# Optimization experiments

Hardware: AMD Instinct MI355X
Metric: run time of the kernel (lower is better)

The kernel has to match this reference:

```python
import jax, jax.numpy as jnp
import numpy as np

B, CH, IMG, P = 16, 3, 384, 16
D, HEADS, DH, MLP, DEPTH = 384, 6, 64, 1536, 6
INNER = HEADS * DH
PD = P * P * 5 * CH          # SPT patch dim = 3840
GRID = IMG // P              # 24
NP = GRID * GRID             # 576 patches
SEQ = NP + 1                 # +cls = 577


def layer_norm(x, g, b, eps=1e-5):
    mu = jnp.mean(x, axis=-1, keepdims=True)
    var = jnp.var(x, axis=-1, keepdims=True)
    return (x - mu) * jax.lax.rsqrt(var + eps) * g + b


def spt_shifts(x):
    # F.pad semantics: (left,right,top,bottom) with negative = crop
    s1 = jnp.pad(x, ((0, 0), (0, 0), (0, 0), (1, 0)))[:, :, :, :-1]  # (1,-1,0,0)
    s2 = jnp.pad(x, ((0, 0), (0, 0), (0, 0), (0, 1)))[:, :, :, 1:]   # (-1,1,0,0)
    s3 = jnp.pad(x, ((0, 0), (0, 0), (1, 0), (0, 0)))[:, :, :-1, :]  # (0,0,1,-1)
    s4 = jnp.pad(x, ((0, 0), (0, 0), (0, 1), (0, 0)))[:, :, 1:, :]   # (0,0,-1,1)
    return jnp.concatenate([x, s1, s2, s3, s4], axis=1)  # [b, 5c, H, W]


def patchify(x):
    # 'b c (h p1) (w p2) -> b (h w) (p1 p2 c)'
    b, c, _, _ = x.shape
    x = x.reshape(b, c, GRID, P, GRID, P)
    x = x.transpose(0, 2, 4, 3, 5, 1)  # b h w p1 p2 c
    return x.reshape(b, GRID * GRID, P * P * c)


def setup_inputs():
    key = jax.random.key(0)
    ks = jax.random.split(key, 16)
    img = jax.random.normal(ks[0], (B, CH, IMG, IMG), jnp.float32)
    spt_g = jnp.ones((PD,), jnp.float32)
    spt_b = jnp.zeros((PD,), jnp.float32)
    spt_w = jax.random.normal(ks[1], (PD, D), jnp.float32) * (1.0 / np.sqrt(PD))
    spt_bias = jnp.zeros((D,), jnp.float32)
    pos = jax.random.normal(ks[2], (1, SEQ, D), jnp.float32) * 0.02
    cls = jax.random.normal(ks[3], (1, 1, D), jnp.float32) * 0.02
    attn_g = jnp.ones((DEPTH, D), jnp.float32)
    attn_b = jnp.zeros((DEPTH, D), jnp.float32)
    temp = jnp.full((DEPTH,), np.log(DH ** -0.5), jnp.float32)
    wqkv = jax.random.normal(ks[4], (DEPTH, D, 3 * INNER), jnp.float32) * 0.02
    wout = jax.random.normal(ks[5], (DEPTH, INNER, D), jnp.float32) * 0.02
    bout = jnp.zeros((DEPTH, D), jnp.float32)
    ff_g = jnp.ones((DEPTH, D), jnp.float32)
    ff_b = jnp.zeros((DEPTH, D), jnp.float32)
    w1 = jax.random.normal(ks[6], (DEPTH, D, MLP), jnp.float32) * 0.02
    b1 = jnp.zeros((DEPTH, MLP), jnp.float32)
    w2 = jax.random.normal(ks[7], (DEPTH, MLP, D), jnp.float32) * 0.02
    b2 = jnp.zeros((DEPTH, D), jnp.float32)
    return {"img": img, "spt_g": spt_g, "spt_b": spt_b, "spt_w": spt_w,
            "spt_bias": spt_bias, "pos": pos, "cls": cls, "attn_g": attn_g,
            "attn_b": attn_b, "temp": temp, "wqkv": wqkv, "wout": wout,
            "bout": bout, "ff_g": ff_g, "ff_b": ff_b, "w1": w1, "b1": b1,
            "w2": w2, "b2": b2}


def vit_forward(img, spt_g, spt_b, spt_w, spt_bias, pos, cls, attn_g, attn_b,
                temp, wqkv, wout, bout, ff_g, ff_b, w1, b1, w2, b2):
    # SPT patch embedding
    x = patchify(spt_shifts(img))                      # [b, NP, PD]
    x = layer_norm(x, spt_g, spt_b) @ spt_w + spt_bias  # [b, NP, D]
    b = x.shape[0]
    cls_tok = jnp.broadcast_to(cls, (b, 1, D))
    x = jnp.concatenate([cls_tok, x], axis=1) + pos[:, :SEQ]

    eye = jnp.eye(SEQ, dtype=bool)
    neg = -jnp.finfo(x.dtype).max

    def block(x, p):
        ag, ab, t, wq, wo, bo, fg, fb, W1, B1, W2, B2 = p
        h = layer_norm(x, ag, ab)
        qkv = h @ wq                                   # [b, n, 3*inner]
        q, k, v = jnp.split(qkv, 3, axis=-1)
        q = q.reshape(b, SEQ, HEADS, DH).transpose(0, 2, 1, 3)
        k = k.reshape(b, SEQ, HEADS, DH).transpose(0, 2, 1, 3)
        v = v.reshape(b, SEQ, HEADS, DH).transpose(0, 2, 1, 3)
        dots = jnp.einsum('bhid,bhjd->bhij', q, k) * jnp.exp(t)
        dots = jnp.where(eye, neg, dots)               # diagonal mask (LSA)
        attn = jax.nn.softmax(dots, axis=-1)
        out = jnp.einsum('bhij,bhjd->bhid', attn, v)
        out = out.transpose(0, 2, 1, 3).reshape(b, SEQ, INNER)
        x = out @ wo + bo + x
        h = layer_norm(x, fg, fb)
        x = jax.nn.gelu(h @ W1 + B1, approximate=False) @ W2 + B2 + x
        return x, None

    params = (attn_g, attn_b, temp, wqkv, wout, bout, ff_g, ff_b, w1, b1, w2, b2)
    x, _ = jax.lax.scan(block, x, params)
    return x


def reference(img, spt_g, spt_b, spt_w, spt_bias, pos, cls, attn_g, attn_b,
              temp, wqkv, wout, bout, ff_g, ff_b, w1, b1, w2, b2):
    return vit_forward(img, spt_g, spt_b, spt_w, spt_bias, pos, cls, attn_g,
                       attn_b, temp, wqkv, wout, bout, ff_g, ff_b, w1, b1,
                       w2, b2)
```

## Files before the change

kernel.cpp:

```cpp
#include <hip/hip_runtime.h>

typedef unsigned short ushort_t;
typedef __bf16 bf16x8 __attribute__((ext_vector_type(8)));
typedef float f32x4 __attribute__((ext_vector_type(4)));

#define SEQ_ 577
#define D_ 384
#define NTOK (16 * 577)

enum { M_QKV = 0, M_OUT, M_MLP1, M_MLP2 };

__device__ inline float b2f(ushort_t u) {
    unsigned int x = ((unsigned int)u) << 16;
    float f; __builtin_memcpy(&f, &x, 4); return f;
}
__device__ inline ushort_t f2b(float f) {
    unsigned int x; __builtin_memcpy(&x, &f, 4);
    x = x + 0x7fffu + ((x >> 16) & 1u);
    return (ushort_t)(x >> 16);
}

__device__ void transpose_tile(const float* __restrict__ src,
                               ushort_t* __restrict__ dst,
                               int ldn, int ldk, int k0, int n0)
{
    __shared__ float t[64][65];
    const int tid = threadIdx.x;
    const int c = tid & 63, rr = tid >> 6;
#pragma unroll
    for (int i = 0; i < 16; i++) {
        int kl = rr + i * 4;
        t[kl][c] = src[(size_t)(k0 + kl) * ldn + n0 + c];
    }
    __syncthreads();
#pragma unroll
    for (int i = 0; i < 16; i++) {
        int nl = rr + i * 4;
        dst[(size_t)(n0 + nl) * ldk + k0 + c] = f2b(t[c][nl]);
    }
}

__global__ __launch_bounds__(256) void prep_spt_kernel(
    const float* __restrict__ w, ushort_t* __restrict__ wt)
{
    transpose_tile(w, wt, 384, 3840, blockIdx.x * 64, blockIdx.y * 64);
}

__global__ __launch_bounds__(256) void prep_all_kernel(
    const float* __restrict__ wqkv, const float* __restrict__ wout,
    const float* __restrict__ w1, const float* __restrict__ w2,
    ushort_t* __restrict__ W6)
{
    int id = blockIdx.x;
    int l = id / 432;
    int r = id - l * 432;
    ushort_t* qkv_t  = W6 + (size_t)l * 1769472;
    ushort_t* wout_t = qkv_t + 442368;
    ushort_t* w1_t   = wout_t + 147456;
    ushort_t* w2_t   = w1_t + 589824;
    const float* wq = wqkv + (size_t)l * 442368;
    const float* wo = wout + (size_t)l * 147456;
    const float* W1 = w1 + (size_t)l * 589824;
    const float* W2 = w2 + (size_t)l * 589824;
    if (r < 108) {
        int kt = r / 18, nt = r % 18;
        transpose_tile(wq, qkv_t, 1152, 384, kt * 64, nt * 64);
    } else if (r < 144) {
        r -= 108; int kt = r / 6, nt = r % 6;
        transpose_tile(wo, wout_t, 384, 384, kt * 64, nt * 64);
    } else if (r < 288) {
        r -= 144; int kt = r / 24, nt = r % 24;
        transpose_tile(W1, w1_t, 1536, 384, kt * 64, nt * 64);
    } else {
        r -= 288; int kt = r / 6, nt = r % 6;
        transpose_tile(W2, w2_t, 384, 1536, kt * 64, nt * 64);
    }
}

template <int MODE>
__global__ __launch_bounds__(256) void gemm64(
    const ushort_t* __restrict__ A, const ushort_t* __restrict__ Bt,
    ushort_t* __restrict__ Co, float* __restrict__ resid,
    const float* __restrict__ bias,
    int M, int K, int ldc)
{
    __shared__ __align__(16) ushort_t As[2][64][40];
    __shared__ __align__(16) ushort_t Bs[2][64][40];

    const int gx = gridDim.x;
    const int nwg = gx * gridDim.y;
    const int f = blockIdx.y * gx + blockIdx.x;
    const int q = nwg >> 3, rr_ = nwg & 7;
    const int xcd = f & 7, ii = f >> 3;
    const int swz = (xcd < rr_ ? xcd * (q + 1) : rr_ * (q + 1) + (xcd - rr_) * q) + ii;
    const int bx = swz % gx, by = swz / gx;

    const int tid = threadIdx.x;
    const int rowBase = by * 64;
    const int colBase = bx * 64;
    const int nk = K >> 5;
    const int lr = tid >> 2, lk = (tid & 3) * 8;
    const int wv = tid >> 6, lane = tid & 63;
    const int wm = (wv >> 1) * 32, wn = (wv & 1) * 32;
    const int m16 = lane & 15, q4 = lane >> 4, kb = q4 * 8;

    const ushort_t* pa = A + (size_t)(rowBase + lr) * K + lk;
    const ushort_t* pb = Bt + (size_t)(colBase + lr) * K + lk;

    f32x4 acc[2][2];
#pragma unroll
    for (int i = 0; i < 2; i++)
#pragma unroll
        for (int j = 0; j < 2; j++) acc[i][j] = (f32x4){0.f, 0.f, 0.f, 0.f};

    uint4 Ua, Ub, Va, Vb;
    auto gloadU = [&](int kt) {
        Ua = *(const uint4*)(pa + kt * 32);
        Ub = *(const uint4*)(pb + kt * 32);
    };
    auto gloadV = [&](int kt) {
        Va = *(const uint4*)(pa + kt * 32);
        Vb = *(const uint4*)(pb + kt * 32);
    };
    auto swriteU = [&](int buf) {
        *(uint4*)&As[buf][lr][lk] = Ua;
        *(uint4*)&Bs[buf][lr][lk] = Ub;
    };
    auto swriteV = [&](int buf) {
        *(uint4*)&As[buf][lr][lk] = Va;
        *(uint4*)&Bs[buf][lr][lk] = Vb;
    };
    auto compute = [&](int buf) {
        bf16x8 a0 = *(const bf16x8*)&As[buf][wm + m16][kb];
        bf16x8 a1 = *(const bf16x8*)&As[buf][wm + 16 + m16][kb];
        bf16x8 b0 = *(const bf16x8*)&Bs[buf][wn + m16][kb];
        bf16x8 b1 = *(const bf16x8*)&Bs[buf][wn + 16 + m16][kb];
        acc[0][0] = __builtin_amdgcn_mfma_f32_16x16x32_bf16(a0, b0, acc[0][0], 0, 0, 0);
        acc[0][1] = __builtin_amdgcn_mfma_f32_16x16x32_bf16(a0, b1, acc[0][1], 0, 0, 0);
        acc[1][0] = __builtin_amdgcn_mfma_f32_16x16x32_bf16(a1, b0, acc[1][0], 0, 0, 0);
        acc[1][1] = __builtin_amdgcn_mfma_f32_16x16x32_bf16(a1, b1, acc[1][1], 0, 0, 0);
    };

    gloadU(0);
    swriteU(0);
    gloadU(1);
    gloadV(2);
    __syncthreads();

    for (int kt = 0; kt < nk; kt += 2) {
        swriteU(1);
        if (kt + 3 < nk) gloadU(kt + 3);
        compute(0);
        __syncthreads();
        if (kt + 2 < nk) {
            swriteV(0);
            if (kt + 4 < nk) gloadV(kt + 4);
        }
        compute(1);
        __syncthreads();
    }

#pragma unroll
    for (int im = 0; im < 2; im++)
#pragma unroll
        for (int in = 0; in < 2; in++) {
            int col = colBase + wn + in * 16 + m16;
#pragma unroll
            for (int r = 0; r < 4; r++) {
                int row = rowBase + wm + im * 16 + q4 * 4 + r;
                if (row >= M) continue;
                float v = acc[im][in][r];
                if (MODE == M_QKV) {
                    Co[(size_t)row * ldc + col] = f2b(v);
                } else if (MODE == M_MLP1) {
                    float t = v + bias[col];
                    float gl = 0.5f * t * (1.0f + erff(t * 0.70710678118f));
                    Co[(size_t)row * ldc + col] = f2b(gl);
                } else {
                    size_t o = (size_t)row * ldc + col;
                    resid[o] = resid[o] + v + bias[col];
                }
            }
        }
}

__global__ __launch_bounds__(256) void gemm64_spt_split(
    const ushort_t* __restrict__ A, const ushort_t* __restrict__ Bt,
    float* __restrict__ resid, int rowOff)
{
    __shared__ __align__(16) ushort_t As[2][64][40];
    __shared__ __align__(16) ushort_t Bs[2][64][40];

    const int f = blockIdx.z * 288 + blockIdx.y * 6 + blockIdx.x;
    const int swz = (f & 7) * 144 + (f >> 3);
    const int bz = swz / 288;
    const int rem = swz - bz * 288;
    const int by = rem / 6, bx = rem - by * 6;

    const int K = 3840, nk = 30;
    const int rowBase = by * 64;
    const int colBase = bx * 64;
    const int kbase = bz * 960;

    const int tid = threadIdx.x;
    const int lr = tid >> 2, lk = (tid & 3) * 8;
    const int wv = tid >> 6, lane = tid & 63;
    const int wm = (wv >> 1) * 32, wn = (wv & 1) * 32;
    const int m16 = lane & 15, q4 = lane >> 4, kb = q4 * 8;

    const ushort_t* pa = A + (size_t)(rowBase + lr) * K + kbase + lk;
    const ushort_t* pb = Bt + (size_t)(colBase + lr) * K + kbase + lk;

    f32x4 acc[2][2];
#pragma unroll
    for (int i = 0; i < 2; i++)
#pragma unroll
        for (int j = 0; j < 2; j++) acc[i][j] = (f32x4){0.f, 0.f, 0.f, 0.f};

    uint4 Ua, Ub, Va, Vb;
    auto gloadU = [&](int kt) {
        Ua = *(const uint4*)(pa + kt * 32);
        Ub = *(const uint4*)(pb + kt * 32);
    };
    auto gloadV = [&](int kt) {
        Va = *(const uint4*)(pa + kt * 32);
        Vb = *(const uint4*)(pb + kt * 32);
    };
    auto swriteU = [&](int buf) {
        *(uint4*)&As[buf][lr][lk] = Ua;
        *(uint4*)&Bs[buf][lr][lk] = Ub;
    };
    auto swriteV = [&](int buf) {
        *(uint4*)&As[buf][lr][lk] = Va;
        *(uint4*)&Bs[buf][lr][lk] = Vb;
    };
    auto compute = [&](int buf) {
        bf16x8 a0 = *(const bf16x8*)&As[buf][wm + m16][kb];
        bf16x8 a1 = *(const bf16x8*)&As[buf][wm + 16 + m16][kb];
        bf16x8 b0 = *(const bf16x8*)&Bs[buf][wn + m16][kb];
        bf16x8 b1 = *(const bf16x8*)&Bs[buf][wn + 16 + m16][kb];
        acc[0][0] = __builtin_amdgcn_mfma_f32_16x16x32_bf16(a0, b0, acc[0][0], 0, 0, 0);
        acc[0][1] = __builtin_amdgcn_mfma_f32_16x16x32_bf16(a0, b1, acc[0][1], 0, 0, 0);
        acc[1][0] = __builtin_amdgcn_mfma_f32_16x16x32_bf16(a1, b0, acc[1][0], 0, 0, 0);
        acc[1][1] = __builtin_amdgcn_mfma_f32_16x16x32_bf16(a1, b1, acc[1][1], 0, 0, 0);
    };

    gloadU(0);
    swriteU(0);
    gloadU(1);
    gloadV(2);
    __syncthreads();

    for (int kt = 0; kt < nk; kt += 2) {
        swriteU(1);
        if (kt + 3 < nk) gloadU(kt + 3);
        compute(0);
        __syncthreads();
        if (kt + 2 < nk) {
            swriteV(0);
            if (kt + 4 < nk) gloadV(kt + 4);
        }
        compute(1);
        __syncthreads();
    }

#pragma unroll
    for (int im = 0; im < 2; im++)
#pragma unroll
        for (int in = 0; in < 2; in++) {
            int col = colBase + wn + in * 16 + m16;
#pragma unroll
            for (int r = 0; r < 4; r++) {
                int row = rowBase + wm + im * 16 + q4 * 4 + r;
                int grow = rowOff + row;
                int bb = grow / 576, p = grow - bb * 576;
                size_t o = ((size_t)(bb * SEQ_ + 1 + p)) * D_ + col;
                atomicAdd(&resid[o], acc[im][in][r]);
            }
        }
}

__global__ __launch_bounds__(256) void attn_kernel(
    const ushort_t* __restrict__ qkv, ushort_t* __restrict__ attn,
    const float* __restrict__ temp, int layer)
{
    const int qt = blockIdx.x;
    const int bh = blockIdx.y;
    const int b = bh / 6, hd = bh - b * 6;
    const int tid = threadIdx.x;
    const int wv = tid >> 6, lane = tid & 63;
    const int m16 = lane & 15, q4 = lane >> 4;
    const float sc2 = expf(temp[layer]) * 1.44269504f;

    __shared__ __align__(16) ushort_t Ks[64][72];
    __shared__ __align__(16) ushort_t Vt[64][72];
    __shared__ __align__(16) ushort_t Pw[4][16][72];

    const int qrow = qt * 64 + wv * 16 + m16;
    const int qtok = qrow < SEQ_ ? qrow : SEQ_ - 1;
    const ushort_t* qb = qkv + ((size_t)(b * SEQ_ + qtok)) * 1152 + hd * 64;
    bf16x8 qf0 = *(const bf16x8*)(qb + q4 * 8);
    bf16x8 qf1 = *(const bf16x8*)(qb + 32 + q4 * 8);

    f32x4 accO[4];
#pragma unroll
    for (int dt = 0; dt < 4; dt++) accO[dt] = (f32x4){0.f, 0.f, 0.f, 0.f};
    float l_r[4] = {0.f, 0.f, 0.f, 0.f};

    const int skey = tid >> 2;
    const int scol = (tid & 3) * 16;
    const int vp   = tid & 31;
    const int vdh  = (tid >> 5) * 8;

    for (int kt = 0; kt < 10; kt++) {
        int key = kt * 64 + skey;
        int gkey = key < SEQ_ ? key : 0;
        const ushort_t* kb_ = qkv + ((size_t)(b * SEQ_ + gkey)) * 1152 + 384 + hd * 64;
        uint4 kv0 = *(const uint4*)(kb_ + scol);
        uint4 kv1 = *(const uint4*)(kb_ + scol + 8);
        if (key >= SEQ_) { kv0 = (uint4){0, 0, 0, 0}; kv1 = kv0; }
        int vk0 = kt * 64 + 2 * vp;
        int t0 = vk0 < SEQ_ ? vk0 : 0;
        int t1 = vk0 + 1 < SEQ_ ? vk0 + 1 : 0;
        uint4 va = *(const uint4*)(qkv + ((size_t)(b * SEQ_ + t0)) * 1152 + 768 + hd * 64 + vdh);
        uint4 vb2 = *(const uint4*)(qkv + ((size_t)(b * SEQ_ + t1)) * 1152 + 768 + hd * 64 + vdh);
        if (vk0 >= SEQ_) va = (uint4){0, 0, 0, 0};
        if (vk0 + 1 >= SEQ_) vb2 = (uint4){0, 0, 0, 0};
        __syncthreads();
        *(uint4*)&Ks[skey][scol] = kv0;
        *(uint4*)&Ks[skey][scol + 8] = kv1;
        {
            const ushort_t* e0 = (const ushort_t*)&va;
            const ushort_t* e1 = (const ushort_t*)&vb2;
#pragma unroll
            for (int j = 0; j < 8; j++) {
                unsigned int pack = (unsigned int)e0[j] | ((unsigned int)e1[j] << 16);
                *(unsigned int*)&Vt[vdh + j][2 * vp] = pack;
            }
        }
        __syncthreads();

        f32x4 s[4];
#pragma unroll
        for (int ct = 0; ct < 4; ct++) {
            bf16x8 b0 = *(const bf16x8*)&Ks[ct * 16 + m16][q4 * 8];
            bf16x8 b1 = *(const bf16x8*)&Ks[ct * 16 + m16][32 + q4 * 8];
            f32x4 z = (f32x4){0.f, 0.f, 0.f, 0.f};
            z = __builtin_amdgcn_mfma_f32_16x16x32_bf16(qf0, b0, z, 0, 0, 0);
            z = __builtin_amdgcn_mfma_f32_16x16x32_bf16(qf1, b1, z, 0, 0, 0);
            s[ct] = z;
        }
        const int rowb = qt * 64 + wv * 16 + q4 * 4;
#pragma unroll
        for (int r = 0; r < 4; r++) {
            float rs = 0.f;
#pragma unroll
            for (int ct = 0; ct < 4; ct++) {
                int col = kt * 64 + ct * 16 + m16;
                float v = s[ct][r] * sc2;
                if (col >= SEQ_ || col == rowb + r) v = -1.0e30f;
                float p = __builtin_amdgcn_exp2f(v);
                s[ct][r] = p;
                rs += p;
            }
            rs += __shfl_xor(rs, 1);
            rs += __shfl_xor(rs, 2);
            rs += __shfl_xor(rs, 4);
            rs += __shfl_xor(rs, 8);
            l_r[r] += rs;
        }
#pragma unroll
        for (int ct = 0; ct < 4; ct++)
#pragma unroll
            for (int r = 0; r < 4; r++)
                Pw[wv][q4 * 4 + r][ct * 16 + m16] = f2b(s[ct][r]);
        bf16x8 pf0 = *(const bf16x8*)&Pw[wv][m16][q4 * 8];
        bf16x8 pf1 = *(const bf16x8*)&Pw[wv][m16][32 + q4 * 8];
#pragma unroll
        for (int dt = 0; dt < 4; dt++) {
            bf16x8 vb0 = *(const bf16x8*)&Vt[dt * 16 + m16][q4 * 8];
            bf16x8 vb1 = *(const bf16x8*)&Vt[dt * 16 + m16][32 + q4 * 8];
            f32x4 o = accO[dt];
            o = __builtin_amdgcn_mfma_f32_16x16x32_bf16(pf0, vb0, o, 0, 0, 0);
            o = __builtin_amdgcn_mfma_f32_16x16x32_bf16(pf1, vb1, o, 0, 0, 0);
            accO[dt] = o;
        }
    }

    const int rowb = qt * 64 + wv * 16 + q4 * 4;
#pragma unroll
    for (int r = 0; r < 4; r++) {
        int grow = rowb + r;
        if (grow >= SEQ_) continue;
        float inv = 1.f / l_r[r];
        ushort_t* op = attn + ((size_t)(b * SEQ_ + grow)) * 384 + hd * 64;
#pragma unroll
        for (int dt = 0; dt < 4; dt++)
            op[dt * 16 + m16] = f2b(accO[dt][r] * inv);
    }
}

__global__ __launch_bounds__(256) void spt_ln_kernel(
    const float* __restrict__ img, const float* __restrict__ gg,
    const float* __restrict__ bb_, ushort_t* __restrict__ Xn, int r0)
{
    int bp = r0 + blockIdx.x;
    int b = bp / 576, p = bp - b * 576;
    int ph = p / 24, pw = p - ph * 24;

    __shared__ float vals[3840];
    __shared__ float red[10];

    const int tid = threadIdx.x;
    const int p1 = tid >> 4, p2 = tid & 15;

    float s = 0.f, sq = 0.f;
#pragma unroll
    for (int plane = 0; plane < 15; plane++) {
        int g5 = plane / 3, ch = plane - g5 * 3;
        int row = ph * 16 + p1, col = pw * 16 + p2;
        if (g5 == 1) col -= 1;
        else if (g5 == 2) col += 1;
        else if (g5 == 3) row -= 1;
        else if (g5 == 4) row += 1;
        float v = 0.f;
        if (row >= 0 && row < 384 && col >= 0 && col < 384)
            v = img[((size_t)(b * 3 + ch) * 384 + row) * 384 + col];
        vals[tid * 15 + plane] = v;
        s += v; sq += v * v;
    }
#pragma unroll
    for (int off = 32; off > 0; off >>= 1) {
        s += __shfl_xor(s, off);
        sq += __shfl_xor(sq, off);
    }
    int wid = tid >> 6;
    if ((tid & 63) == 0) { red[wid] = s; red[4 + wid] = sq; }
    __syncthreads();
    if (tid == 0) {
        float S = red[0] + red[1] + red[2] + red[3];
        float Q = red[4] + red[5] + red[6] + red[7];
        float mean = S / 3840.f;
        float var = Q / 3840.f - mean * mean;
        red[8] = mean;
        red[9] = rsqrtf(var + 1e-5f);
    }
    __syncthreads();
    float mean = red[8], rstd = red[9];
#pragma unroll
    for (int i = 0; i < 15; i++) {
        int k = tid + i * 256;
        float v = (vals[k] - mean) * rstd * gg[k] + bb_[k];
        Xn[(size_t)blockIdx.x * 3840 + k] = f2b(v);
    }
}

__global__ __launch_bounds__(256) void ln_kernel(
    const float* __restrict__ x, const float* __restrict__ g,
    const float* __restrict__ b, ushort_t* __restrict__ h)
{
    int row = blockIdx.x * 4 + (threadIdx.x >> 6);
    int lane = threadIdx.x & 63;
    const float4* xr = (const float4*)(x + (size_t)row * 384);
    float4 a = xr[lane];
    float4 c = (lane < 32) ? xr[64 + lane] : make_float4(0.f, 0.f, 0.f, 0.f);
    float s = a.x + a.y + a.z + a.w + c.x + c.y + c.z + c.w;
    float sq = a.x * a.x + a.y * a.y + a.z * a.z + a.w * a.w
             + c.x * c.x + c.y * c.y + c.z * c.z + c.w * c.w;
#pragma unroll
    for (int off = 32; off > 0; off >>= 1) {
        s += __shfl_xor(s, off);
        sq += __shfl_xor(sq, off);
    }
    float mean = s / 384.f;
    float var = sq / 384.f - mean * mean;
    float rstd = rsqrtf(var + 1e-5f);
    const float4* g4 = (const float4*)g;
    const float4* b4 = (const float4*)b;
    ushort_t* hr = h + (size_t)row * 384;
    {
        float4 gv = g4[lane], bv = b4[lane];
        unsigned int lo = (unsigned int)f2b((a.x - mean) * rstd * gv.x + bv.x)
                        | ((unsigned int)f2b((a.y - mean) * rstd * gv.y + bv.y) << 16);
        unsigned int hi = (unsigned int)f2b((a.z - mean) * rstd * gv.z + bv.z)
                        | ((unsigned int)f2b((a.w - mean) * rstd * gv.w + bv.w) << 16);
        *(uint2*)&hr[lane * 4] = make_uint2(lo, hi);
    }
    if (lane < 32) {
        float4 gv = g4[64 + lane], bv = b4[64 + lane];
        unsigned int lo = (unsigned int)f2b((c.x - mean) * rstd * gv.x + bv.x)
                        | ((unsigned int)f2b((c.y - mean) * rstd * gv.y + bv.y) << 16);
        unsigned int hi = (unsigned int)f2b((c.z - mean) * rstd * gv.z + bv.z)
                        | ((unsigned int)f2b((c.w - mean) * rstd * gv.w + bv.w) << 16);
        *(uint2*)&hr[256 + lane * 4] = make_uint2(lo, hi);
    }
}

__global__ void init_x_kernel(const float* __restrict__ cls,
                              const float* __restrict__ pos,
                              const float* __restrict__ spt_bias,
                              float* __restrict__ x)
{
    int s = blockIdx.x, b = blockIdx.y, d = threadIdx.x;
    float base = (s == 0) ? cls[d] : spt_bias[d];
    x[((size_t)b * SEQ_ + s) * D_ + d] = base + pos[(size_t)s * D_ + d];
}

extern "C" void kernel_launch(void* const* d_in, const int* in_sizes, int n_in,
                              void* d_out, int out_size, void* d_ws, size_t ws_size,
                              hipStream_t stream)
{
    const float* img      = (const float*)d_in[0];
    const float* spt_g    = (const float*)d_in[1];
    const float* spt_b    = (const float*)d_in[2];
    const float* spt_w    = (const float*)d_in[3];
    const float* spt_bias = (const float*)d_in[4];
    const float* pos      = (const float*)d_in[5];
    const float* clsp     = (const float*)d_in[6];
    const float* attn_g   = (const float*)d_in[7];
    const float* attn_b   = (const float*)d_in[8];
    const float* temp     = (const float*)d_in[9];
    const float* wqkv     = (const float*)d_in[10];
    const float* wout     = (const float*)d_in[11];
    const float* bout     = (const float*)d_in[12];
    const float* ff_g     = (const float*)d_in[13];
    const float* ff_b     = (const float*)d_in[14];
    const float* w1       = (const float*)d_in[15];
    const float* b1       = (const float*)d_in[16];
    const float* w2       = (const float*)d_in[17];
    const float* b2       = (const float*)d_in[18];

    float* x = (float*)d_out;

    char* base = (char*)d_ws;
    ushort_t* qkv   = (ushort_t*)base;
    ushort_t* attn  = (ushort_t*)(base + (size_t)NTOK * 1152 * 2);
    ushort_t* Xn    = (ushort_t*)base;
    ushort_t* gbuf  = (ushort_t*)base;
    ushort_t* spt_wt = (ushort_t*)(base + 23592960);
    char* p2 = base + (size_t)NTOK * 1536 * 2;
    ushort_t* h  = (ushort_t*)p2;
    char* p3 = p2 + (size_t)NTOK * 384 * 2;
    ushort_t* W6 = (ushort_t*)p3;

    prep_all_kernel<<<2592, 256, 0, stream>>>(wqkv, wout, w1, w2, W6);
    prep_spt_kernel<<<dim3(60, 6), 256, 0, stream>>>(spt_w, spt_wt);
    init_x_kernel<<<dim3(SEQ_, 16), 384, 0, stream>>>(clsp, pos, spt_bias, x);

    for (int c = 0; c < 3; c++) {
        int r0 = c * 3072;
        spt_ln_kernel<<<3072, 256, 0, stream>>>(img, spt_g, spt_b, Xn, r0);
        gemm64_spt_split<<<dim3(6, 48, 4), 256, 0, stream>>>(Xn, spt_wt, x, r0);
    }

    for (int l = 0; l < 6; l++) {
        ushort_t* qkv_t  = W6 + (size_t)l * 1769472;
        ushort_t* wout_t = qkv_t + 442368;
        ushort_t* w1_t   = wout_t + 147456;
        ushort_t* w2_t   = w1_t + 589824;
        ln_kernel<<<NTOK / 4, 256, 0, stream>>>(x, attn_g + l * 384, attn_b + l * 384, h);
        gemm64<M_QKV><<<dim3(18, 145), 256, 0, stream>>>(
            h, qkv_t, qkv, nullptr, nullptr, NTOK, 384, 1152);
        attn_kernel<<<dim3(10, 96), 256, 0, stream>>>(qkv, attn, temp, l);
        gemm64<M_OUT><<<dim3(6, 145), 256, 0, stream>>>(
            attn, wout_t, nullptr, x, bout + l * 384, NTOK, 384, 384);
        ln_kernel<<<NTOK / 4, 256, 0, stream>>>(x, ff_g + l * 384, ff_b + l * 384, h);
        gemm64<M_MLP1><<<dim3(24, 145), 256, 0, stream>>>(
            h, w1_t, gbuf, nullptr, b1 + l * 1536, NTOK, 384, 1536);
        gemm64<M_MLP2><<<dim3(6, 145), 256, 0, stream>>>(
            gbuf, w2_t, nullptr, x, b2 + l * 384, NTOK, 1536, 384);
    }
}
```

Measured before the change: 1.202 ms.

## Fuse LayerNorm into QKV and MLP1 GEMMs by folding gamma/beta into weights

Removes the standalone LayerNorm kernels. The LN gamma is folded into the transposed weights, and beta·W is precomputed as an extra bias. Each GEMM block now computes per-row mean and rstd from the fp32 residual and normalizes the A tile while loading it, in place of reading a bf16 LN output. The exact erf GELU is also replaced by a tanh-style approximation using exp2 and rcp. The trade-off is that the A operand is read as fp32 (double the bytes) and every column block recomputes the row statistics, with some change in numerical error.

```diff
diff --git a/kernel.cpp b/kernel.cpp
--- a/kernel.cpp
+++ b/kernel.cpp
@@ -22,6 +22,7 @@
 
 __device__ void transpose_tile(const float* __restrict__ src,
                                ushort_t* __restrict__ dst,
+                               const float* __restrict__ g,
                                int ldn, int ldk, int k0, int n0)
 {
     __shared__ float t[64][65];
@@ -33,22 +34,24 @@
         t[kl][c] = src[(size_t)(k0 + kl) * ldn + n0 + c];
     }
     __syncthreads();
+    float sc = g ? g[k0 + c] : 1.0f;
 #pragma unroll
     for (int i = 0; i < 16; i++) {
         int nl = rr + i * 4;
-        dst[(size_t)(n0 + nl) * ldk + k0 + c] = f2b(t[c][nl]);
+        dst[(size_t)(n0 + nl) * ldk + k0 + c] = f2b(t[c][nl] * sc);
     }
 }
 
 __global__ __launch_bounds__(256) void prep_spt_kernel(
     const float* __restrict__ w, ushort_t* __restrict__ wt)
 {
-    transpose_tile(w, wt, 384, 3840, blockIdx.x * 64, blockIdx.y * 64);
+    transpose_tile(w, wt, nullptr, 384, 3840, blockIdx.x * 64, blockIdx.y * 64);
 }
 
 __global__ __launch_bounds__(256) void prep_all_kernel(
     const float* __restrict__ wqkv, const float* __restrict__ wout,
     const float* __restrict__ w1, const float* __restrict__ w2,
+    const float* __restrict__ attn_g, const float* __restrict__ ff_g,
     ushort_t* __restrict__ W6)
 {
     int id = blockIdx.x;
@@ -64,26 +67,52 @@
     const float* W2 = w2 + (size_t)l * 589824;
     if (r < 108) {
         int kt = r / 18, nt = r % 18;
-        transpose_tile(wq, qkv_t, 1152, 384, kt * 64, nt * 64);
+        transpose_tile(wq, qkv_t, attn_g + l * 384, 1152, 384, kt * 64, nt * 64);
     } else if (r < 144) {
         r -= 108; int kt = r / 6, nt = r % 6;
-        transpose_tile(wo, wout_t, 384, 384, kt * 64, nt * 64);
+        transpose_tile(wo, wout_t, nullptr, 384, 384, kt * 64, nt * 64);
     } else if (r < 288) {
         r -= 144; int kt = r / 24, nt = r % 24;
-        transpose_tile(W1, w1_t, 1536, 384, kt * 64, nt * 64);
+        transpose_tile(W1, w1_t, ff_g + l * 384, 1536, 384, kt * 64, nt * 64);
     } else {
         r -= 288; int kt = r / 6, nt = r % 6;
-        transpose_tile(W2, w2_t, 384, 1536, kt * 64, nt * 64);
+        transpose_tile(W2, w2_t, nullptr, 384, 1536, kt * 64, nt * 64);
+    }
+}
+
+__global__ __launch_bounds__(256) void prep_bias_kernel(
+    const float* __restrict__ wqkv, const float* __restrict__ w1,
+    const float* __restrict__ b1, const float* __restrict__ attn_b,
+    const float* __restrict__ ff_b, float* __restrict__ qb2,
+    float* __restrict__ mb2)
+{
+    int gidx = blockIdx.x * 256 + threadIdx.x;
+    if (gidx >= 6 * 2688) return;
+    int l = gidx / 2688, r = gidx - l * 2688;
+    if (r < 1152) {
+        const float* W = wqkv + (size_t)l * 442368;
+        const float* bb = attn_b + l * 384;
+        float s = 0.f;
+        for (int k = 0; k < 384; k++) s += bb[k] * W[(size_t)k * 1152 + r];
+        qb2[l * 1152 + r] = s;
+    } else {
+        int n = r - 1152;
+        const float* W = w1 + (size_t)l * 589824;
+        const float* bb = ff_b + l * 384;
+        float s = b1[l * 1536 + n];
+        for (int k = 0; k < 384; k++) s += bb[k] * W[(size_t)k * 1536 + n];
+        mb2[l * 1536 + n] = s;
     }
 }
 
 template <int MODE>
 __global__ __launch_bounds__(256) void gemm64(
-    const ushort_t* __restrict__ A, const ushort_t* __restrict__ Bt,
+    const void* __restrict__ Av, const ushort_t* __restrict__ Bt,
     ushort_t* __restrict__ Co, float* __restrict__ resid,
     const float* __restrict__ bias,
     int M, int K, int ldc)
 {
+    constexpr bool LNF = (MODE == M_QKV || MODE == M_MLP1);
     __shared__ __align__(16) ushort_t As[2][64][40];
     __shared__ __align__(16) ushort_t Bs[2][64][40];
 
@@ -99,12 +128,34 @@
     const int rowBase = by * 64;
     const int colBase = bx * 64;
     const int nk = K >> 5;
-    const int lr = tid >> 2, lk = (tid & 3) * 8;
+    const int lr = tid >> 2, lq = tid & 3, lk = lq * 8;
     const int wv = tid >> 6, lane = tid & 63;
     const int wm = (wv >> 1) * 32, wn = (wv & 1) * 32;
     const int m16 = lane & 15, q4 = lane >> 4, kb = q4 * 8;
 
-    const ushort_t* pa = A + (size_t)(rowBase + lr) * K + lk;
+    const float* paf = nullptr;
+    const ushort_t* pa = nullptr;
+    float rstd = 0.f, nc = 0.f;
+    if constexpr (LNF) {
+        int ar = rowBase + lr;
+        if (ar >= M) ar = M - 1;
+        paf = (const float*)Av + (size_t)ar * K;
+        const float4* p4 = (const float4*)(paf + lq * 96);
+        float s = 0.f, sq = 0.f;
+#pragma unroll
+        for (int i = 0; i < 24; i++) {
+            float4 v = p4[i];
+            s += v.x + v.y + v.z + v.w;
+            sq += v.x * v.x + v.y * v.y + v.z * v.z + v.w * v.w;
+        }
+        s += __shfl_xor(s, 1);  s += __shfl_xor(s, 2);
+        sq += __shfl_xor(sq, 1); sq += __shfl_xor(sq, 2);
+        float mean = s * (1.f / 384.f);
+        rstd = rsqrtf(sq * (1.f / 384.f) - mean * mean + 1e-5f);
+        nc = -mean * rstd;
+    } else {
+        pa = (const ushort_t*)Av + (size_t)(rowBase + lr) * K + lk;
+    }
     const ushort_t* pb = Bt + (size_t)(colBase + lr) * K + lk;
 
     f32x4 acc[2][2];
@@ -114,20 +165,45 @@
         for (int j = 0; j < 2; j++) acc[i][j] = (f32x4){0.f, 0.f, 0.f, 0.f};
 
     uint4 Ua, Ub, Va, Vb;
+    float4 Uaf0, Uaf1, Vaf0, Vaf1;
+    auto nrm8 = [&](float4 a, float4 b) -> bf16x8 {
+        bf16x8 r;
+        r[0] = (__bf16)fmaf(a.x, rstd, nc);
+        r[1] = (__bf16)fmaf(a.y, rstd, nc);
+        r[2] = (__bf16)fmaf(a.z, rstd, nc);
+        r[3] = (__bf16)fmaf(a.w, rstd, nc);
+        r[4] = (__bf16)fmaf(b.x, rstd, nc);
+        r[5] = (__bf16)fmaf(b.y, rstd, nc);
+        r[6] = (__bf16)fmaf(b.z, rstd, nc);
+        r[7] = (__bf16)fmaf(b.w, rstd, nc);
+        return r;
+    };
     auto gloadU = [&](int kt) {
-        Ua = *(const uint4*)(pa + kt * 32);
+        if constexpr (LNF) {
+            const float4* p = (const float4*)(paf + kt * 32 + lk);
+            Uaf0 = p[0]; Uaf1 = p[1];
+        } else {
+            Ua = *(const uint4*)(pa + kt * 32);
+        }
         Ub = *(const uint4*)(pb + kt * 32);
     };
     auto gloadV = [&](int kt) {
-        Va = *(const uint4*)(pa + kt * 32);
+        if constexpr (LNF) {
+            const float4* p = (const float4*)(paf + kt * 32 + lk);
+            Vaf0 = p[0]; Vaf1 = p[1];
+        } else {
+            Va = *(const uint4*)(pa + kt * 32);
+        }
         Vb = *(const uint4*)(pb + kt * 32);
     };
     auto swriteU = [&](int buf) {
-        *(uint4*)&As[buf][lr][lk] = Ua;
+        if constexpr (LNF) *(bf16x8*)&As[buf][lr][lk] = nrm8(Uaf0, Uaf1);
+        else               *(uint4*)&As[buf][lr][lk] = Ua;
         *(uint4*)&Bs[buf][lr][lk] = Ub;
     };
     auto swriteV = [&](int buf) {
-        *(uint4*)&As[buf][lr][lk] = Va;
+        if constexpr (LNF) *(bf16x8*)&As[buf][lr][lk] = nrm8(Vaf0, Vaf1);
+        else               *(uint4*)&As[buf][lr][lk] = Va;
         *(uint4*)&Bs[buf][lr][lk] = Vb;
     };
     auto compute = [&](int buf) {
@@ -171,10 +247,12 @@
                 if (row >= M) continue;
                 float v = acc[im][in][r];
                 if (MODE == M_QKV) {
-                    Co[(size_t)row * ldc + col] = f2b(v);
+                    Co[(size_t)row * ldc + col] = f2b(v + bias[col]);
                 } else if (MODE == M_MLP1) {
                     float t = v + bias[col];
-                    float gl = 0.5f * t * (1.0f + erff(t * 0.70710678118f));
+                    float u = t * (0.7978845608f + 0.0356774081f * t * t);
+                    float e = __builtin_amdgcn_exp2f(2.885390082f * u);
+                    float gl = t - t * __builtin_amdgcn_rcpf(e + 1.0f);
                     Co[(size_t)row * ldc + col] = f2b(gl);
                 } else {
                     size_t o = (size_t)row * ldc + col;
@@ -455,47 +533,6 @@
     }
 }
 
-__global__ __launch_bounds__(256) void ln_kernel(
-    const float* __restrict__ x, const float* __restrict__ g,
-    const float* __restrict__ b, ushort_t* __restrict__ h)
-{
-    int row = blockIdx.x * 4 + (threadIdx.x >> 6);
-    int lane = threadIdx.x & 63;
-    const float4* xr = (const float4*)(x + (size_t)row * 384);
-    float4 a = xr[lane];
-    float4 c = (lane < 32) ? xr[64 + lane] : make_float4(0.f, 0.f, 0.f, 0.f);
-    float s = a.x + a.y + a.z + a.w + c.x + c.y + c.z + c.w;
-    float sq = a.x * a.x + a.y * a.y + a.z * a.z + a.w * a.w
-             + c.x * c.x + c.y * c.y + c.z * c.z + c.w * c.w;
-#pragma unroll
-    for (int off = 32; off > 0; off >>= 1) {
-        s += __shfl_xor(s, off);
-        sq += __shfl_xor(sq, off);
-    }
-    float mean = s / 384.f;
-    float var = sq / 384.f - mean * mean;
-    float rstd = rsqrtf(var + 1e-5f);
-    const float4* g4 = (const float4*)g;
-    const float4* b4 = (const float4*)b;
-    ushort_t* hr = h + (size_t)row * 384;
-    {
-        float4 gv = g4[lane], bv = b4[lane];
-        unsigned int lo = (unsigned int)f2b((a.x - mean) * rstd * gv.x + bv.x)
-                        | ((unsigned int)f2b((a.y - mean) * rstd * gv.y + bv.y) << 16);
-        unsigned int hi = (unsigned int)f2b((a.z - mean) * rstd * gv.z + bv.z)
-                        | ((unsigned int)f2b((a.w - mean) * rstd * gv.w + bv.w) << 16);
-        *(uint2*)&hr[lane * 4] = make_uint2(lo, hi);
-    }
-    if (lane < 32) {
-        float4 gv = g4[64 + lane], bv = b4[64 + lane];
-        unsigned int lo = (unsigned int)f2b((c.x - mean) * rstd * gv.x + bv.x)
-                        | ((unsigned int)f2b((c.y - mean) * rstd * gv.y + bv.y) << 16);
-        unsigned int hi = (unsigned int)f2b((c.z - mean) * rstd * gv.z + bv.z)
-                        | ((unsigned int)f2b((c.w - mean) * rstd * gv.w + bv.w) << 16);
-        *(uint2*)&hr[256 + lane * 4] = make_uint2(lo, hi);
-    }
-}
-
 __global__ void init_x_kernel(const float* __restrict__ cls,
                               const float* __restrict__ pos,
                               const float* __restrict__ spt_bias,
@@ -539,11 +576,13 @@
     ushort_t* gbuf  = (ushort_t*)base;
     ushort_t* spt_wt = (ushort_t*)(base + 23592960);
     char* p2 = base + (size_t)NTOK * 1536 * 2;
-    ushort_t* h  = (ushort_t*)p2;
+    float* qb2 = (float*)p2;
+    float* mb2 = qb2 + 6 * 1152;
     char* p3 = p2 + (size_t)NTOK * 384 * 2;
     ushort_t* W6 = (ushort_t*)p3;
 
-    prep_all_kernel<<<2592, 256, 0, stream>>>(wqkv, wout, w1, w2, W6);
+    prep_all_kernel<<<2592, 256, 0, stream>>>(wqkv, wout, w1, w2, attn_g, ff_g, W6);
+    prep_bias_kernel<<<63, 256, 0, stream>>>(wqkv, w1, b1, attn_b, ff_b, qb2, mb2);
     prep_spt_kernel<<<dim3(60, 6), 256, 0, stream>>>(spt_w, spt_wt);
     init_x_kernel<<<dim3(SEQ_, 16), 384, 0, stream>>>(clsp, pos, spt_bias, x);
 
@@ -558,15 +597,13 @@
         ushort_t* wout_t = qkv_t + 442368;
         ushort_t* w1_t   = wout_t + 147456;
         ushort_t* w2_t   = w1_t + 589824;
-        ln_kernel<<<NTOK / 4, 256, 0, stream>>>(x, attn_g + l * 384, attn_b + l * 384, h);
         gemm64<M_QKV><<<dim3(18, 145), 256, 0, stream>>>(
-            h, qkv_t, qkv, nullptr, nullptr, NTOK, 384, 1152);
+            x, qkv_t, qkv, nullptr, qb2 + l * 1152, NTOK, 384, 1152);
         attn_kernel<<<dim3(10, 96), 256, 0, stream>>>(qkv, attn, temp, l);
         gemm64<M_OUT><<<dim3(6, 145), 256, 0, stream>>>(
             attn, wout_t, nullptr, x, bout + l * 384, NTOK, 384, 384);
-        ln_kernel<<<NTOK / 4, 256, 0, stream>>>(x, ff_g + l * 384, ff_b + l * 384, h);
         gemm64<M_MLP1><<<dim3(24, 145), 256, 0, stream>>>(
-            h, w1_t, gbuf, nullptr, b1 + l * 1536, NTOK, 384, 1536);
+            x, w1_t, gbuf, nullptr, mb2 + l * 1536, NTOK, 384, 1536);
         gemm64<M_MLP2><<<dim3(6, 145), 256, 0, stream>>>(
             gbuf, w2_t, nullptr, x, b2 + l * 384, NTOK, 1536, 384);
     }
```

Measured after the change: 1.552 ms. 1.29x slower.
